# Kernel optimization log

Hardware: AMD Instinct MI355X
Metric: run time of the kernel (lower is better)

The kernel has to match this reference:

```python
import jax, jax.numpy as jnp
import numpy as np

B, T, D, E, H = 8, 2048, 1024, 8, 256
LN_EPS = 1e-5  # torch.nn.LayerNorm default


def setup_inputs() -> dict:
    key = jax.random.key(0)
    ks = jax.random.split(key, 4)
    return {
        "x": jax.random.normal(ks[0], (B, T, D), dtype=jnp.float32),
        "Wg": jax.random.normal(ks[1], (E, D), dtype=jnp.float32) * 0.02,
        "ln_scale": jnp.ones((E, D), dtype=jnp.float32),
        "ln_bias": jnp.zeros((E, D), dtype=jnp.float32),
        "W1": jax.random.normal(ks[2], (E, D, H), dtype=jnp.float32) * 0.02,
        "b1": jnp.zeros((E, H), dtype=jnp.float32),
        "W2": jax.random.normal(ks[3], (E, H, D), dtype=jnp.float32) * 0.02,
        "b2": jnp.zeros((E, D), dtype=jnp.float32),
    }


def reference(x, Wg, ln_scale, ln_bias, W1, b1, W2, b2):
    Bs, Ts, Ds = x.shape
    xt = x.reshape(Bs * Ts, Ds)                      # [N, D]
    logits = xt @ Wg.T                               # [N, E]
    # softmax is monotone, so argmax(softmax(logits)) == argmax(logits)
    top1 = jnp.argmax(logits, axis=-1)               # [N] int

    # LayerNorm normalization is expert-independent; compute once.
    mu = jnp.mean(xt, axis=-1, keepdims=True)
    var = jnp.mean(jnp.square(xt - mu), axis=-1, keepdims=True)
    xhat = (xt - mu) * jax.lax.rsqrt(var + LN_EPS)   # [N, D]

    n_experts = Wg.shape[0]

    def body(y, p):
        s_e, b_e, w1, bb1, w2, bb2, eid = p
        h = jax.nn.gelu((xhat * s_e + b_e) @ w1 + bb1, approximate=False)  # [N, H]
        out = h @ w2 + bb2                                                  # [N, D]
        mask = (top1 == eid)[:, None].astype(out.dtype)
        return y + mask * out, None

    y0 = jnp.zeros_like(xt)
    y, _ = jax.lax.scan(
        body, y0, (ln_scale, ln_bias, W1, b1, W2, b2, jnp.arange(n_experts))
    )
    # dropout p=0.0 is identity
    return y.reshape(Bs, Ts, Ds)
```

## Files before the change

### kernel.cpp

```cpp
#include <hip/hip_runtime.h>
#include <hip/hip_bf16.h>
#include <math.h>

#define N_TOK 16384
#define D_DIM 1024
#define E_NUM 8
#define H_DIM 256
#define LN_EPS 1e-5f

#define BM 128
#define BN 128
#define BN1 64
#define BK 32
#define MAXTILES (N_TOK / BM + E_NUM)
#define MP (MAXTILES * BM)

typedef __attribute__((ext_vector_type(8))) short bf16x8;
typedef __attribute__((ext_vector_type(4))) float f32x4;

__device__ __forceinline__ unsigned short f2bf(float f) {
  union { float f; unsigned u; } cv; cv.f = f;
  unsigned u = cv.u;
  u += 0x7fffu + ((u >> 16) & 1u);
  return (unsigned short)(u >> 16);
}

__device__ __forceinline__ void gl_lds16(const void* g, void* l) {
  __builtin_amdgcn_global_load_lds(
      (const __attribute__((address_space(1))) unsigned int*)g,
      (__attribute__((address_space(3))) unsigned int*)l, 16, 0, 0);
}

__global__ __launch_bounds__(256) void smoe_gate(
    const float* __restrict__ x, const float* __restrict__ wg,
    const float* __restrict__ ln_s, const float* __restrict__ ln_b,
    unsigned short* __restrict__ xhat, int* __restrict__ eid)
{
  int lane = threadIdx.x & 63, wave = threadIdx.x >> 6;
  int t = blockIdx.x * 4 + wave;

  const float4* x4 = (const float4*)x + (size_t)t * 256;
  float4 v[4];
  float s = 0.f, ss = 0.f;
#pragma unroll
  for (int j = 0; j < 4; j++) {
    v[j] = x4[lane + 64 * j];
    s  += v[j].x + v[j].y + v[j].z + v[j].w;
    ss += v[j].x * v[j].x + v[j].y * v[j].y + v[j].z * v[j].z + v[j].w * v[j].w;
  }
  const float4* wg4 = (const float4*)wg;
  double lg[E_NUM];
#pragma unroll
  for (int e = 0; e < E_NUM; e++) {
    double acc = 0.0;
#pragma unroll
    for (int j = 0; j < 4; j++) {
      float4 w = wg4[e * 256 + lane + 64 * j];
      acc += (double)v[j].x * w.x + (double)v[j].y * w.y
           + (double)v[j].z * w.z + (double)v[j].w * w.w;
    }
    lg[e] = acc;
  }

  double a0, a1, a2, a3;
  {
    double p0 = __shfl_xor(lg[0], 1, 64), p1 = __shfl_xor(lg[1], 1, 64);
    double p2 = __shfl_xor(lg[2], 1, 64), p3 = __shfl_xor(lg[3], 1, 64);
    double p4 = __shfl_xor(lg[4], 1, 64), p5 = __shfl_xor(lg[5], 1, 64);
    double p6 = __shfl_xor(lg[6], 1, 64), p7 = __shfl_xor(lg[7], 1, 64);
    bool b = lane & 1;
    a0 = b ? lg[1] + p1 : lg[0] + p0;
    a1 = b ? lg[3] + p3 : lg[2] + p2;
    a2 = b ? lg[5] + p5 : lg[4] + p4;
    a3 = b ? lg[7] + p7 : lg[6] + p6;
  }
  double c0, c1;
  {
    double q0 = __shfl_xor(a0, 2, 64), q1 = __shfl_xor(a1, 2, 64);
    double q2 = __shfl_xor(a2, 2, 64), q3 = __shfl_xor(a3, 2, 64);
    bool b = (lane >> 1) & 1;
    c0 = b ? a1 + q1 : a0 + q0;
    c1 = b ? a3 + q3 : a2 + q2;
  }
  double c;
  {
    double r0 = __shfl_xor(c0, 4, 64), r1 = __shfl_xor(c1, 4, 64);
    bool b = (lane >> 2) & 1;
    c = b ? c1 + r1 : c0 + r0;
  }
  c += __shfl_xor(c, 8, 64);
  c += __shfl_xor(c, 16, 64);
  c += __shfl_xor(c, 32, 64);

  double val = c; int idx = lane & 7;
#pragma unroll
  for (int m = 1; m < E_NUM; m <<= 1) {
    double ov = __shfl_xor(val, m, 64);
    int    oi = __shfl_xor(idx, m, 64);
    if (ov > val || (ov == val && oi < idx)) { val = ov; idx = oi; }
  }
  int best = idx;

#pragma unroll
  for (int m = 1; m < 64; m <<= 1) {
    s  += __shfl_xor(s, m, 64);
    ss += __shfl_xor(ss, m, 64);
  }
  float mean = s * (1.0f / (float)D_DIM);
  float var  = ss * (1.0f / (float)D_DIM) - mean * mean;
  float rstd = 1.0f / sqrtf(var + LN_EPS);

  if (lane == 0) eid[t] = best;

  const float4* s4 = (const float4*)(ln_s + (size_t)best * D_DIM);
  const float4* b4 = (const float4*)(ln_b + (size_t)best * D_DIM);
  ushort4* xo = (ushort4*)(xhat + (size_t)t * D_DIM);
#pragma unroll
  for (int j = 0; j < 4; j++) {
    float4 sc = s4[lane + 64 * j], bi = b4[lane + 64 * j];
    ushort4 o;
    o.x = f2bf((v[j].x - mean) * rstd * sc.x + bi.x);
    o.y = f2bf((v[j].y - mean) * rstd * sc.y + bi.y);
    o.z = f2bf((v[j].z - mean) * rstd * sc.z + bi.z);
    o.w = f2bf((v[j].w - mean) * rstd * sc.w + bi.w);
    xo[lane + 64 * j] = o;
  }
}

__global__ __launch_bounds__(1024) void smoe_route(
    const int* __restrict__ eid, int* __restrict__ texp, int* __restrict__ tokp)
{
  int tid = threadIdx.x;
  int lane = tid & 63, wave = tid >> 6;

  int cnt[E_NUM] = {};
  int ee[16];
#pragma unroll
  for (int j = 0; j < 16; j++) {
    int e = eid[j * 1024 + tid];
    ee[j] = e;
#pragma unroll
    for (int k = 0; k < E_NUM; k++) cnt[k] += (e == k);
  }
  int inc[E_NUM];
#pragma unroll
  for (int k = 0; k < E_NUM; k++) inc[k] = cnt[k];
#pragma unroll
  for (int m = 1; m < 64; m <<= 1) {
#pragma unroll
    for (int k = 0; k < E_NUM; k++) {
      int o = __shfl_up(inc[k], m, 64);
      if (lane >= m) inc[k] += o;
    }
  }
  __shared__ int wtot[16][E_NUM];
  __shared__ int wbase[16][E_NUM];
  __shared__ int ebase[E_NUM];
  __shared__ int ecnt[E_NUM];
  __shared__ int epad[E_NUM];
  if (lane == 63)
#pragma unroll
    for (int k = 0; k < E_NUM; k++) wtot[wave][k] = inc[k];
  __syncthreads();
  if (tid == 0) {
    int run[E_NUM] = {};
    for (int w = 0; w < 16; w++)
#pragma unroll
      for (int k = 0; k < E_NUM; k++) { wbase[w][k] = run[k]; run[k] += wtot[w][k]; }
    int b = 0, ti = 0;
    for (int k = 0; k < E_NUM; k++) {
      ecnt[k] = run[k];
      ebase[k] = b;
      int nt = (run[k] + BM - 1) / BM;
      for (int j = 0; j < nt; j++) texp[ti++] = k;
      epad[k] = nt * BM;
      b += nt * BM;
    }
    for (; ti < MAXTILES; ti++) texp[ti] = -1;
  }
  __syncthreads();
  int tb[E_NUM];
#pragma unroll
  for (int k = 0; k < E_NUM; k++) tb[k] = wbase[wave][k] + inc[k] - cnt[k];
  int run2[E_NUM] = {};
#pragma unroll
  for (int j = 0; j < 16; j++) {
    int e = ee[j];
    int r = 0;
#pragma unroll
    for (int k = 0; k < E_NUM; k++) {
      if (e == k) r = tb[k] + run2[k];
      run2[k] += (e == k);
    }
    tokp[ebase[e] + r] = j * 1024 + tid;
  }
#pragma unroll
  for (int k = 0; k < E_NUM; k++) {
    int s0 = ebase[k] + ecnt[k], n = epad[k] - ecnt[k];
    for (int i = tid; i < n; i += 1024) tokp[s0 + i] = -1;
  }
}

__global__ __launch_bounds__(256) void smoe_cvt2(
    const float* __restrict__ w1, unsigned short* __restrict__ w1t,
    const float* __restrict__ w2, unsigned short* __restrict__ w2t)
{
  int bid = blockIdx.x;
  const float* in; unsigned short* out; int R, C;
  if (bid < 2048) { in = w1; out = w1t; R = D_DIM; C = H_DIM; }
  else            { in = w2; out = w2t; R = H_DIM; C = D_DIM; bid -= 2048; }
  int rt = R / 32, ct = C / 32;
  int e = bid / (rt * ct);
  int rem = bid % (rt * ct);
  int r0 = (rem / ct) * 32, c0 = (rem % ct) * 32;
  __shared__ float tile[32][33];
  int tx = threadIdx.x & 31, ty = threadIdx.x >> 5;
  const float* src = in + (size_t)e * R * C;
#pragma unroll
  for (int i = 0; i < 4; i++)
    tile[ty + 8 * i][tx] = src[(size_t)(r0 + ty + 8 * i) * C + c0 + tx];
  __syncthreads();
  unsigned short* dst = out + (size_t)e * R * C;
#pragma unroll
  for (int i = 0; i < 4; i++)
    dst[(size_t)(c0 + ty + 8 * i) * R + r0 + tx] = f2bf(tile[tx][ty + 8 * i]);
}

__global__ __launch_bounds__(256) void smoe_gemm1(
    const unsigned short* __restrict__ xhat,
    const unsigned short* __restrict__ w1t,
    const float* __restrict__ b1,
    const int* __restrict__ texp,
    const int* __restrict__ tokp,
    unsigned short* __restrict__ hbuf)
{
  int mt = blockIdx.x;
  int e = texp[mt];
  if (e < 0) return;
  int nt = blockIdx.y;
  int tid = threadIdx.x;
  __shared__ unsigned short As[BM * BK];
  __shared__ unsigned short Bs[BN1 * BK];
  int r = tid >> 2;
  int c = tid & 3;
  int row0 = mt * BM + r, row1 = row0 + 64;
  int tok0 = tokp[row0]; tok0 = tok0 < 0 ? 0 : tok0;
  int tok1 = tokp[row1]; tok1 = tok1 < 0 ? 0 : tok1;
  const unsigned short* a0 = xhat + (size_t)tok0 * D_DIM + c * 8;
  const unsigned short* a1 = xhat + (size_t)tok1 * D_DIM + c * 8;
  const unsigned short* bb = w1t + (size_t)e * H_DIM * D_DIM
                           + (size_t)(nt * BN1 + r) * D_DIM + c * 8;
  unsigned short* As0 = As + r * BK + c * 8;
  unsigned short* As1 = As + (r + 64) * BK + c * 8;
  unsigned short* Bs0 = Bs + r * BK + c * 8;

  int wave = tid >> 6, lane = tid & 63;
  int wr = (wave >> 1) * 64;
  int wc = (wave & 1) * 32;
  int qm = lane & 15;
  int quad = lane >> 4;
  f32x4 acc[4][2] = {};

  for (int k0 = 0; k0 < D_DIM; k0 += BK) {
    gl_lds16(a0 + k0, As0);
    gl_lds16(a1 + k0, As1);
    gl_lds16(bb + k0, Bs0);
    __syncthreads();
    bf16x8 af[4], bf[2];
#pragma unroll
    for (int i = 0; i < 4; i++)
      af[i] = *(const bf16x8*)(As + (wr + i * 16 + qm) * BK + quad * 8);
#pragma unroll
    for (int i = 0; i < 2; i++)
      bf[i] = *(const bf16x8*)(Bs + (wc + i * 16 + qm) * BK + quad * 8);
#pragma unroll
    for (int mi = 0; mi < 4; mi++)
#pragma unroll
      for (int ni = 0; ni < 2; ni++)
        acc[mi][ni] = __builtin_amdgcn_mfma_f32_16x16x32_bf16(
            af[mi], bf[ni], acc[mi][ni], 0, 0, 0);
    __syncthreads();
  }
  int mbase = mt * BM;
#pragma unroll
  for (int ni = 0; ni < 2; ni++) {
    int col = nt * BN1 + wc + ni * 16 + qm;
    float bias = b1[e * H_DIM + col];
#pragma unroll
    for (int mi = 0; mi < 4; mi++) {
      int rl = wr + mi * 16 + quad * 4;
#pragma unroll
      for (int i = 0; i < 4; i++) {
        float vv = acc[mi][ni][i] + bias;
        float g = 0.5f * vv * (1.0f + erff(vv * 0.70710678118654752f));
        hbuf[(size_t)(mbase + rl + i) * H_DIM + col] = f2bf(g);
      }
    }
  }
}

__global__ __launch_bounds__(256) void smoe_gemm2(
    const unsigned short* __restrict__ hbuf,
    const unsigned short* __restrict__ w2t,
    const float* __restrict__ b2,
    const int* __restrict__ texp,
    const int* __restrict__ tokp,
    float* __restrict__ y)
{
  int mt = blockIdx.x;
  int e = texp[mt];
  if (e < 0) return;
  int nt = blockIdx.y;
  int tid = threadIdx.x;
  __shared__ unsigned short As[BM * BK];
  __shared__ unsigned short Bs[BN * BK];
  int r = tid >> 2;
  int c = tid & 3;
  const unsigned short* a0 = hbuf + (size_t)(mt * BM + r) * H_DIM + c * 8;
  const unsigned short* a1 = a0 + (size_t)64 * H_DIM;
  const unsigned short* bb = w2t + (size_t)e * D_DIM * H_DIM
                           + (size_t)(nt * BN + r) * H_DIM + c * 8;
  const unsigned short* bb1 = bb + (size_t)64 * H_DIM;
  unsigned short* As0 = As + r * BK + c * 8;
  unsigned short* As1 = As + (r + 64) * BK + c * 8;
  unsigned short* Bs0 = Bs + r * BK + c * 8;
  unsigned short* Bs1 = Bs + (r + 64) * BK + c * 8;

  int wave = tid >> 6, lane = tid & 63;
  int wr = (wave >> 1) * 64;
  int wc = (wave & 1) * 64;
  int qm = lane & 15;
  int quad = lane >> 4;
  f32x4 acc[4][4] = {};

  for (int k0 = 0; k0 < H_DIM; k0 += BK) {
    gl_lds16(a0 + k0, As0);
    gl_lds16(a1 + k0, As1);
    gl_lds16(bb + k0, Bs0);
    gl_lds16(bb1 + k0, Bs1);
    __syncthreads();
    bf16x8 af[4], bf[4];
#pragma unroll
    for (int i = 0; i < 4; i++) {
      af[i] = *(const bf16x8*)(As + (wr + i * 16 + qm) * BK + quad * 8);
      bf[i] = *(const bf16x8*)(Bs + (wc + i * 16 + qm) * BK + quad * 8);
    }
#pragma unroll
    for (int mi = 0; mi < 4; mi++)
#pragma unroll
      for (int ni = 0; ni < 4; ni++)
        acc[mi][ni] = __builtin_amdgcn_mfma_f32_16x16x32_bf16(
            af[mi], bf[ni], acc[mi][ni], 0, 0, 0);
    __syncthreads();
  }
  int mbase = mt * BM;
#pragma unroll
  for (int mi = 0; mi < 4; mi++) {
#pragma unroll
    for (int i = 0; i < 4; i++) {
      int row = mbase + wr + mi * 16 + quad * 4 + i;
      int tok = tokp[row];
      if (tok < 0) continue;
#pragma unroll
      for (int ni = 0; ni < 4; ni++) {
        int col = nt * BN + wc + ni * 16 + qm;
        y[(size_t)tok * D_DIM + col] = acc[mi][ni][i] + b2[e * D_DIM + col];
      }
    }
  }
}

extern "C" void kernel_launch(void* const* d_in, const int* in_sizes, int n_in,
                              void* d_out, int out_size, void* d_ws, size_t ws_size,
                              hipStream_t stream) {
  (void)in_sizes; (void)n_in; (void)out_size; (void)ws_size;
  const float* x    = (const float*)d_in[0];
  const float* wg   = (const float*)d_in[1];
  const float* ln_s = (const float*)d_in[2];
  const float* ln_b = (const float*)d_in[3];
  const float* w1   = (const float*)d_in[4];
  const float* b1   = (const float*)d_in[5];
  const float* w2   = (const float*)d_in[6];
  const float* b2   = (const float*)d_in[7];
  float* y = (float*)d_out;

  char* ws = (char*)d_ws;
  size_t off = 0;
  auto alloc = [&](size_t bytes) {
    void* p = ws + off;
    off = (off + bytes + 255) & ~(size_t)255;
    return p;
  };
  unsigned short* xhat = (unsigned short*)alloc((size_t)N_TOK * D_DIM * 2);
  unsigned short* w1t  = (unsigned short*)alloc((size_t)E_NUM * D_DIM * H_DIM * 2);
  unsigned short* w2t  = (unsigned short*)alloc((size_t)E_NUM * D_DIM * H_DIM * 2);
  unsigned short* hbuf = (unsigned short*)alloc((size_t)MP * H_DIM * 2);
  int* eid    = (int*)alloc((size_t)N_TOK * 4);
  int* tokp   = (int*)alloc((size_t)MP * 4);
  int* texp   = (int*)alloc((size_t)MAXTILES * 4);

  smoe_gate<<<N_TOK / 4, 256, 0, stream>>>(x, wg, ln_s, ln_b, xhat, eid);
  smoe_route<<<1, 1024, 0, stream>>>(eid, texp, tokp);
  smoe_cvt2<<<4096, 256, 0, stream>>>(w1, w1t, w2, w2t);
  smoe_gemm1<<<dim3(MAXTILES, H_DIM / BN1), 256, 0, stream>>>(xhat, w1t, b1, texp, tokp, hbuf);
  smoe_gemm2<<<dim3(MAXTILES, D_DIM / BN), 256, 0, stream>>>(hbuf, w2t, b2, texp, tokp, y);
}
```

Measured before the change: 253.5 us.

## Double-buffer swizzled LDS in expert GEMMs and fuse weight conversion into gate

```diff
diff --git a/kernel.cpp b/kernel.cpp
--- a/kernel.cpp
+++ b/kernel.cpp
@@ -1,5 +1,4 @@
 #include <hip/hip_runtime.h>
-#include <hip/hip_bf16.h>
 #include <math.h>
 
 #define N_TOK 16384
@@ -9,9 +8,8 @@
 #define LN_EPS 1e-5f
 
 #define BM 128
-#define BN 128
 #define BN1 64
-#define BK 32
+#define BKG 64
 #define MAXTILES (N_TOK / BM + E_NUM)
 #define MP (MAXTILES * BM)
 
@@ -31,13 +29,38 @@
       (__attribute__((address_space(3))) unsigned int*)l, 16, 0, 0);
 }
 
-__global__ __launch_bounds__(256) void smoe_gate(
+__global__ __launch_bounds__(256) void smoe_gate_cvt(
     const float* __restrict__ x, const float* __restrict__ wg,
     const float* __restrict__ ln_s, const float* __restrict__ ln_b,
-    unsigned short* __restrict__ xhat, int* __restrict__ eid)
+    unsigned short* __restrict__ xhat, int* __restrict__ eid,
+    const float* __restrict__ w1, unsigned short* __restrict__ w1t,
+    const float* __restrict__ w2, unsigned short* __restrict__ w2t)
 {
+  if (blockIdx.x & 1) {
+    int bid = blockIdx.x >> 1;
+    const float* in; unsigned short* out; int R, C;
+    if (bid < 2048) { in = w1; out = w1t; R = D_DIM; C = H_DIM; }
+    else            { in = w2; out = w2t; R = H_DIM; C = D_DIM; bid -= 2048; }
+    int rt = R / 32, ct = C / 32;
+    int e = bid / (rt * ct);
+    int rem = bid % (rt * ct);
+    int r0 = (rem / ct) * 32, c0 = (rem % ct) * 32;
+    __shared__ float tile[32][33];
+    int tx = threadIdx.x & 31, ty = threadIdx.x >> 5;
+    const float* src = in + (size_t)e * R * C;
+#pragma unroll
+    for (int i = 0; i < 4; i++)
+      tile[ty + 8 * i][tx] = src[(size_t)(r0 + ty + 8 * i) * C + c0 + tx];
+    __syncthreads();
+    unsigned short* dst = out + (size_t)e * R * C;
+#pragma unroll
+    for (int i = 0; i < 4; i++)
+      dst[(size_t)(c0 + ty + 8 * i) * R + r0 + tx] = f2bf(tile[tx][ty + 8 * i]);
+    return;
+  }
+
   int lane = threadIdx.x & 63, wave = threadIdx.x >> 6;
-  int t = blockIdx.x * 4 + wave;
+  int t = (blockIdx.x >> 1) * 4 + wave;
 
   const float4* x4 = (const float4*)x + (size_t)t * 256;
   float4 v[4];
@@ -52,14 +75,20 @@
   double lg[E_NUM];
 #pragma unroll
   for (int e = 0; e < E_NUM; e++) {
-    double acc = 0.0;
-#pragma unroll
-    for (int j = 0; j < 4; j++) {
+    double a0 = 0.0, a1 = 0.0;
+#pragma unroll
+    for (int j = 0; j < 2; j++) {
       float4 w = wg4[e * 256 + lane + 64 * j];
-      acc += (double)v[j].x * w.x + (double)v[j].y * w.y
-           + (double)v[j].z * w.z + (double)v[j].w * w.w;
-    }
-    lg[e] = acc;
+      a0 += (double)v[j].x * w.x + (double)v[j].y * w.y
+          + (double)v[j].z * w.z + (double)v[j].w * w.w;
+    }
+#pragma unroll
+    for (int j = 2; j < 4; j++) {
+      float4 w = wg4[e * 256 + lane + 64 * j];
+      a1 += (double)v[j].x * w.x + (double)v[j].y * w.y
+          + (double)v[j].z * w.z + (double)v[j].w * w.w;
+    }
+    lg[e] = a0 + a1;
   }
 
   double a0, a1, a2, a3;
@@ -199,31 +228,6 @@
     int s0 = ebase[k] + ecnt[k], n = epad[k] - ecnt[k];
     for (int i = tid; i < n; i += 1024) tokp[s0 + i] = -1;
   }
-}
-
-__global__ __launch_bounds__(256) void smoe_cvt2(
-    const float* __restrict__ w1, unsigned short* __restrict__ w1t,
-    const float* __restrict__ w2, unsigned short* __restrict__ w2t)
-{
-  int bid = blockIdx.x;
-  const float* in; unsigned short* out; int R, C;
-  if (bid < 2048) { in = w1; out = w1t; R = D_DIM; C = H_DIM; }
-  else            { in = w2; out = w2t; R = H_DIM; C = D_DIM; bid -= 2048; }
-  int rt = R / 32, ct = C / 32;
-  int e = bid / (rt * ct);
-  int rem = bid % (rt * ct);
-  int r0 = (rem / ct) * 32, c0 = (rem % ct) * 32;
-  __shared__ float tile[32][33];
-  int tx = threadIdx.x & 31, ty = threadIdx.x >> 5;
-  const float* src = in + (size_t)e * R * C;
-#pragma unroll
-  for (int i = 0; i < 4; i++)
-    tile[ty + 8 * i][tx] = src[(size_t)(r0 + ty + 8 * i) * C + c0 + tx];
-  __syncthreads();
-  unsigned short* dst = out + (size_t)e * R * C;
-#pragma unroll
-  for (int i = 0; i < 4; i++)
-    dst[(size_t)(c0 + ty + 8 * i) * R + r0 + tx] = f2bf(tile[tx][ty + 8 * i]);
 }
 
 __global__ __launch_bounds__(256) void smoe_gemm1(
@@ -239,48 +243,80 @@
   if (e < 0) return;
   int nt = blockIdx.y;
   int tid = threadIdx.x;
-  __shared__ unsigned short As[BM * BK];
-  __shared__ unsigned short Bs[BN1 * BK];
-  int r = tid >> 2;
-  int c = tid & 3;
-  int row0 = mt * BM + r, row1 = row0 + 64;
-  int tok0 = tokp[row0]; tok0 = tok0 < 0 ? 0 : tok0;
-  int tok1 = tokp[row1]; tok1 = tok1 < 0 ? 0 : tok1;
-  const unsigned short* a0 = xhat + (size_t)tok0 * D_DIM + c * 8;
-  const unsigned short* a1 = xhat + (size_t)tok1 * D_DIM + c * 8;
-  const unsigned short* bb = w1t + (size_t)e * H_DIM * D_DIM
-                           + (size_t)(nt * BN1 + r) * D_DIM + c * 8;
-  unsigned short* As0 = As + r * BK + c * 8;
-  unsigned short* As1 = As + (r + 64) * BK + c * 8;
-  unsigned short* Bs0 = Bs + r * BK + c * 8;
+  __shared__ unsigned short As[2][BM * BKG];
+  __shared__ unsigned short Bs[2][BN1 * BKG];
+
+  int r8 = tid >> 3;
+  int c8 = tid & 7;
+  int slot = c8 ^ (r8 & 7);
+
+  const unsigned short* asrc[4];
+#pragma unroll
+  for (int j = 0; j < 4; j++) {
+    int row = r8 + 32 * j;
+    int tok = tokp[mt * BM + row];
+    tok = tok < 0 ? 0 : tok;
+    asrc[j] = xhat + (size_t)tok * D_DIM + slot * 8;
+  }
+  const unsigned short* bsrc[2];
+#pragma unroll
+  for (int j = 0; j < 2; j++)
+    bsrc[j] = w1t + (size_t)e * H_DIM * D_DIM
+            + (size_t)(nt * BN1 + r8 + 32 * j) * D_DIM + slot * 8;
 
   int wave = tid >> 6, lane = tid & 63;
   int wr = (wave >> 1) * 64;
   int wc = (wave & 1) * 32;
-  int qm = lane & 15;
-  int quad = lane >> 4;
+  int qm = lane & 15, quad = lane >> 4;
+
+  int arow[4], brow[2], soff[2];
+#pragma unroll
+  for (int mi = 0; mi < 4; mi++) arow[mi] = (wr + mi * 16 + qm) * BKG;
+#pragma unroll
+  for (int ni = 0; ni < 2; ni++) brow[ni] = (wc + ni * 16 + qm) * BKG;
+#pragma unroll
+  for (int kk = 0; kk < 2; kk++) soff[kk] = ((kk * 4 + quad) ^ (qm & 7)) * 8;
+
   f32x4 acc[4][2] = {};
-
-  for (int k0 = 0; k0 < D_DIM; k0 += BK) {
-    gl_lds16(a0 + k0, As0);
-    gl_lds16(a1 + k0, As1);
-    gl_lds16(bb + k0, Bs0);
+  int cur = 0;
+
+#pragma unroll
+  for (int j = 0; j < 4; j++) gl_lds16(asrc[j], &As[0][j * 2048 + tid * 8]);
+#pragma unroll
+  for (int j = 0; j < 2; j++) gl_lds16(bsrc[j], &Bs[0][j * 2048 + tid * 8]);
+  __syncthreads();
+
+  for (int t = 0; t < D_DIM / BKG; ++t) {
+    if (t + 1 < D_DIM / BKG) {
+      int k0 = (t + 1) * BKG;
+      int nb = cur ^ 1;
+#pragma unroll
+      for (int j = 0; j < 4; j++) gl_lds16(asrc[j] + k0, &As[nb][j * 2048 + tid * 8]);
+#pragma unroll
+      for (int j = 0; j < 2; j++) gl_lds16(bsrc[j] + k0, &Bs[nb][j * 2048 + tid * 8]);
+    }
+    bf16x8 af[2][4], bfr[2][2];
+#pragma unroll
+    for (int kk = 0; kk < 2; kk++) {
+#pragma unroll
+      for (int mi = 0; mi < 4; mi++)
+        af[kk][mi] = *(const bf16x8*)&As[cur][arow[mi] + soff[kk]];
+#pragma unroll
+      for (int ni = 0; ni < 2; ni++)
+        bfr[kk][ni] = *(const bf16x8*)&Bs[cur][brow[ni] + soff[kk]];
+    }
+#pragma unroll
+    for (int kk = 0; kk < 2; kk++)
+#pragma unroll
+      for (int mi = 0; mi < 4; mi++)
+#pragma unroll
+        for (int ni = 0; ni < 2; ni++)
+          acc[mi][ni] = __builtin_amdgcn_mfma_f32_16x16x32_bf16(
+              af[kk][mi], bfr[kk][ni], acc[mi][ni], 0, 0, 0);
     __syncthreads();
-    bf16x8 af[4], bf[2];
-#pragma unroll
-    for (int i = 0; i < 4; i++)
-      af[i] = *(const bf16x8*)(As + (wr + i * 16 + qm) * BK + quad * 8);
-#pragma unroll
-    for (int i = 0; i < 2; i++)
-      bf[i] = *(const bf16x8*)(Bs + (wc + i * 16 + qm) * BK + quad * 8);
-#pragma unroll
-    for (int mi = 0; mi < 4; mi++)
-#pragma unroll
-      for (int ni = 0; ni < 2; ni++)
-        acc[mi][ni] = __builtin_amdgcn_mfma_f32_16x16x32_bf16(
-            af[mi], bf[ni], acc[mi][ni], 0, 0, 0);
-    __syncthreads();
-  }
+    cur ^= 1;
+  }
+
   int mbase = mt * BM;
 #pragma unroll
   for (int ni = 0; ni < 2; ni++) {
@@ -312,47 +348,76 @@
   if (e < 0) return;
   int nt = blockIdx.y;
   int tid = threadIdx.x;
-  __shared__ unsigned short As[BM * BK];
-  __shared__ unsigned short Bs[BN * BK];
-  int r = tid >> 2;
-  int c = tid & 3;
-  const unsigned short* a0 = hbuf + (size_t)(mt * BM + r) * H_DIM + c * 8;
-  const unsigned short* a1 = a0 + (size_t)64 * H_DIM;
-  const unsigned short* bb = w2t + (size_t)e * D_DIM * H_DIM
-                           + (size_t)(nt * BN + r) * H_DIM + c * 8;
-  const unsigned short* bb1 = bb + (size_t)64 * H_DIM;
-  unsigned short* As0 = As + r * BK + c * 8;
-  unsigned short* As1 = As + (r + 64) * BK + c * 8;
-  unsigned short* Bs0 = Bs + r * BK + c * 8;
-  unsigned short* Bs1 = Bs + (r + 64) * BK + c * 8;
+  __shared__ unsigned short As[2][BM * BKG];
+  __shared__ unsigned short Bs[2][BN1 * BKG];
+
+  int r8 = tid >> 3;
+  int c8 = tid & 7;
+  int slot = c8 ^ (r8 & 7);
+
+  const unsigned short* asrc[4];
+#pragma unroll
+  for (int j = 0; j < 4; j++)
+    asrc[j] = hbuf + (size_t)(mt * BM + r8 + 32 * j) * H_DIM + slot * 8;
+  const unsigned short* bsrc[2];
+#pragma unroll
+  for (int j = 0; j < 2; j++)
+    bsrc[j] = w2t + (size_t)e * D_DIM * H_DIM
+            + (size_t)(nt * BN1 + r8 + 32 * j) * H_DIM + slot * 8;
 
   int wave = tid >> 6, lane = tid & 63;
   int wr = (wave >> 1) * 64;
-  int wc = (wave & 1) * 64;
-  int qm = lane & 15;
-  int quad = lane >> 4;
-  f32x4 acc[4][4] = {};
-
-  for (int k0 = 0; k0 < H_DIM; k0 += BK) {
-    gl_lds16(a0 + k0, As0);
-    gl_lds16(a1 + k0, As1);
-    gl_lds16(bb + k0, Bs0);
-    gl_lds16(bb1 + k0, Bs1);
+  int wc = (wave & 1) * 32;
+  int qm = lane & 15, quad = lane >> 4;
+
+  int arow[4], brow[2], soff[2];
+#pragma unroll
+  for (int mi = 0; mi < 4; mi++) arow[mi] = (wr + mi * 16 + qm) * BKG;
+#pragma unroll
+  for (int ni = 0; ni < 2; ni++) brow[ni] = (wc + ni * 16 + qm) * BKG;
+#pragma unroll
+  for (int kk = 0; kk < 2; kk++) soff[kk] = ((kk * 4 + quad) ^ (qm & 7)) * 8;
+
+  f32x4 acc[4][2] = {};
+  int cur = 0;
+
+#pragma unroll
+  for (int j = 0; j < 4; j++) gl_lds16(asrc[j], &As[0][j * 2048 + tid * 8]);
+#pragma unroll
+  for (int j = 0; j < 2; j++) gl_lds16(bsrc[j], &Bs[0][j * 2048 + tid * 8]);
+  __syncthreads();
+
+  for (int t = 0; t < H_DIM / BKG; ++t) {
+    if (t + 1 < H_DIM / BKG) {
+      int k0 = (t + 1) * BKG;
+      int nb = cur ^ 1;
+#pragma unroll
+      for (int j = 0; j < 4; j++) gl_lds16(asrc[j] + k0, &As[nb][j * 2048 + tid * 8]);
+#pragma unroll
+      for (int j = 0; j < 2; j++) gl_lds16(bsrc[j] + k0, &Bs[nb][j * 2048 + tid * 8]);
+    }
+    bf16x8 af[2][4], bfr[2][2];
+#pragma unroll
+    for (int kk = 0; kk < 2; kk++) {
+#pragma unroll
+      for (int mi = 0; mi < 4; mi++)
+        af[kk][mi] = *(const bf16x8*)&As[cur][arow[mi] + soff[kk]];
+#pragma unroll
+      for (int ni = 0; ni < 2; ni++)
+        bfr[kk][ni] = *(const bf16x8*)&Bs[cur][brow[ni] + soff[kk]];
+    }
+#pragma unroll
+    for (int kk = 0; kk < 2; kk++)
+#pragma unroll
+      for (int mi = 0; mi < 4; mi++)
+#pragma unroll
+        for (int ni = 0; ni < 2; ni++)
+          acc[mi][ni] = __builtin_amdgcn_mfma_f32_16x16x32_bf16(
+              af[kk][mi], bfr[kk][ni], acc[mi][ni], 0, 0, 0);
     __syncthreads();
-    bf16x8 af[4], bf[4];
-#pragma unroll
-    for (int i = 0; i < 4; i++) {
-      af[i] = *(const bf16x8*)(As + (wr + i * 16 + qm) * BK + quad * 8);
-      bf[i] = *(const bf16x8*)(Bs + (wc + i * 16 + qm) * BK + quad * 8);
-    }
-#pragma unroll
-    for (int mi = 0; mi < 4; mi++)
-#pragma unroll
-      for (int ni = 0; ni < 4; ni++)
-        acc[mi][ni] = __builtin_amdgcn_mfma_f32_16x16x32_bf16(
-            af[mi], bf[ni], acc[mi][ni], 0, 0, 0);
-    __syncthreads();
-  }
+    cur ^= 1;
+  }
+
   int mbase = mt * BM;
 #pragma unroll
   for (int mi = 0; mi < 4; mi++) {
@@ -362,8 +427,8 @@
       int tok = tokp[row];
       if (tok < 0) continue;
 #pragma unroll
-      for (int ni = 0; ni < 4; ni++) {
-        int col = nt * BN + wc + ni * 16 + qm;
+      for (int ni = 0; ni < 2; ni++) {
+        int col = nt * BN1 + wc + ni * 16 + qm;
         y[(size_t)tok * D_DIM + col] = acc[mi][ni][i] + b2[e * D_DIM + col];
       }
     }
@@ -399,9 +464,9 @@
   int* tokp   = (int*)alloc((size_t)MP * 4);
   int* texp   = (int*)alloc((size_t)MAXTILES * 4);
 
-  smoe_gate<<<N_TOK / 4, 256, 0, stream>>>(x, wg, ln_s, ln_b, xhat, eid);
+  smoe_gate_cvt<<<8192, 256, 0, stream>>>(x, wg, ln_s, ln_b, xhat, eid,
+                                          w1, w1t, w2, w2t);
   smoe_route<<<1, 1024, 0, stream>>>(eid, texp, tokp);
-  smoe_cvt2<<<4096, 256, 0, stream>>>(w1, w1t, w2, w2t);
   smoe_gemm1<<<dim3(MAXTILES, H_DIM / BN1), 256, 0, stream>>>(xhat, w1t, b1, texp, tokp, hbuf);
-  smoe_gemm2<<<dim3(MAXTILES, D_DIM / BN), 256, 0, stream>>>(hbuf, w2t, b2, texp, tokp, y);
-}
+  smoe_gemm2<<<dim3(MAXTILES, D_DIM / BN1), 256, 0, stream>>>(hbuf, w2t, b2, texp, tokp, y);
+}
```

Result: slower. 287.3 us (+13.3%).
